# Kernel tuning notes

Measured on AMD Instinct MI355X. Metric: run time of the kernel, lower is better.

## Reference

```python
import jax, jax.numpy as jnp
import numpy as np

B, N, D, YD = 256, 1024, 64, 2
EPS = 1e-7  # keras SCC epsilon clip


def interleave(x):
    # (B, L, ...): out[:,0::2]=first half, out[:,1::2]=second half
    b, L = x.shape[0], x.shape[1]
    a, c = x[:, : L // 2], x[:, L // 2:]
    return jnp.stack([a, c], axis=2).reshape((b, L) + x.shape[2:])


def block_interleave(x, scope):
    # tf.split into N//scope chunks of size `scope`, Interleave each, concat
    b, L = x.shape[0], x.shape[1]
    rest = x.shape[2:]
    xr = x.reshape((b, L // scope, 2, scope // 2) + rest)
    xr = jnp.swapaxes(xr, 2, 3)
    return xr.reshape((b, L) + rest)


def split_even_odd(x):
    # returns (odd, even) = (x[:,0::2], x[:,1::2])
    return x[:, 0::2], x[:, 1::2]


def mlp2(x, W1, b1, W2, b2):
    return jnp.dot(jax.nn.relu(jnp.dot(x, W1) + b1), W2) + b2


def emb2llr(e, W, b):
    return jax.nn.softmax(jnp.dot(e, W) + b, axis=-1)


def scce(v, p):
    # v: (B,L,1) int labels, p: (B,L,2) probs -> (B,L) per-element NLL
    pt = jnp.take_along_axis(p, v, axis=-1)[..., 0]
    return -jnp.log(jnp.clip(pt, EPS, 1.0))


def setup_inputs() -> dict:
    key = jax.random.key(0)
    ks = jax.random.split(key, 16)
    s = lambda fan: 1.0 / np.sqrt(fan)
    return {
        "x": jax.random.randint(ks[0], (B, N, 1), 0, 2, dtype=jnp.int32),
        "y": jax.random.normal(ks[1], (B, N, YD), dtype=jnp.float32),
        "emb_W": jax.random.normal(ks[2], (YD, D), dtype=jnp.float32) * s(YD),
        "emb_b": jnp.zeros((D,), jnp.float32),
        "lab_emb": jax.random.normal(ks[3], (2, D), dtype=jnp.float32) * s(D),
        "cn_W1": jax.random.normal(ks[4], (2 * D, D), dtype=jnp.float32) * s(2 * D),
        "cn_b1": jnp.zeros((D,), jnp.float32),
        "cn_W2": jax.random.normal(ks[5], (D, D), dtype=jnp.float32) * s(D),
        "cn_b2": jnp.zeros((D,), jnp.float32),
        "bn_W1": jax.random.normal(ks[6], (3 * D, D), dtype=jnp.float32) * s(3 * D),
        "bn_b1": jnp.zeros((D,), jnp.float32),
        "bn_W2": jax.random.normal(ks[7], (D, D), dtype=jnp.float32) * s(D),
        "bn_b2": jnp.zeros((D,), jnp.float32),
        "llr_W": jax.random.normal(ks[8], (D, 2), dtype=jnp.float32) * s(D),
        "llr_b": jnp.zeros((2,), jnp.float32),
    }


def reference(x, y, emb_W, emb_b, lab_emb, cn_W1, cn_b1, cn_W2, cn_b2,
              bn_W1, bn_b1, bn_W2, bn_b2, llr_W, llr_b):
    v = x.astype(jnp.int32)  # (B,N,1)
    e = jnp.dot(y, emb_W) + emb_b  # (B,N,D) observation embedding

    losses, preds, norms = [], [], []
    pred = emb2llr(e, llr_W, llr_b)
    losses.append(scce(v, pred))
    preds.append(pred)
    norms.append(jnp.linalg.norm(e, axis=-1))

    scope = 2
    while scope <= N:
        v_il = block_interleave(v, scope)
        v_odd, v_even = split_even_odd(v_il)
        v_xor = jnp.mod(v_odd + v_even, 2)  # (B,N/2,1)
        v_prime = interleave(jnp.concatenate((v_xor, v_even), axis=1))

        e_il = block_interleave(e, scope)
        e_odd, e_even = split_even_odd(e_il)  # (B,N/2,D) each
        v_xor_emb = lab_emb[v_xor[..., 0]]  # (B,N/2,D)

        e1_left = mlp2(jnp.concatenate((e_odd, e_even), axis=-1),
                       cn_W1, cn_b1, cn_W2, cn_b2)
        e1_right = mlp2(jnp.concatenate((e_odd, e_even, v_xor_emb), axis=-1),
                        bn_W1, bn_b1, bn_W2, bn_b2)
        e_prime = interleave(jnp.concatenate((e1_left, e1_right), axis=1))

        pred = emb2llr(e_prime, llr_W, llr_b)
        losses.append(scce(v_prime, pred))
        preds.append(pred)
        norms.append(jnp.linalg.norm(e_prime, axis=-1))

        v, e = v_prime, e_prime
        scope *= 2

    return (jnp.stack(losses, axis=-2),   # (B, S, N)
            jnp.stack(preds, axis=-2),    # (B, N, S, 2)
            jnp.stack(norms, axis=-2))    # (B, S, N)
```

## Files before the change

kernel.cpp:

```cpp
#include <hip/hip_runtime.h>
#include <hip/hip_bf16.h>

#define NB 256
#define NN 1024
#define NSTAGES 11
#define EPSF 1e-7f

typedef unsigned short u16;
typedef unsigned int u32;
typedef unsigned long long u64;
typedef __attribute__((ext_vector_type(8))) short short8;
typedef __attribute__((ext_vector_type(16))) float f32x16;

static constexpr size_t PRED_BASE = (size_t)NB * NSTAGES * NN;
static constexpr size_t NORM_BASE = PRED_BASE + (size_t)NB * NN * NSTAGES * 2;

static constexpr int LW_OFF = 24576;

#define WLDS_FR 30
#define NWREG (48 - WLDS_FR)

static constexpr size_t STAGE_OFF = 131072;
static constexpr size_t PRED_F2_PER_B = (size_t)NSTAGES * NN;

__device__ __forceinline__ u16 f2bf(float f) {
  unsigned u = __float_as_uint(f);
  unsigned r = (u + 0x7fffu + ((u >> 16) & 1u)) >> 16;
  return (u16)r;
}
__device__ __forceinline__ unsigned pack_bf2(float a, float b) {
  __hip_bfloat162 h = __float22bfloat162_rn(make_float2(a, b));
  return *(unsigned*)&h;
}
__device__ __forceinline__ u32 spread16(u32 v) {
  v = (v | (v << 8)) & 0x00FF00FFu;
  v = (v | (v << 4)) & 0x0F0F0F0Fu;
  v = (v | (v << 2)) & 0x33333333u;
  v = (v | (v << 1)) & 0x55555555u;
  return v;
}
template <bool STAGED>
__device__ __forceinline__ void emit_out(float* __restrict__ out, float* __restrict__ pred_ws,
                                         int b, int n, int s,
                                         float z0, float z1, float nrm2, int label) {
  float m  = fmaxf(z0, z1);
  float p0 = expf(z0 - m), p1 = expf(z1 - m);
  float inv = 1.0f / (p0 + p1);
  p0 *= inv; p1 *= inv;
  float pt = label ? p1 : p0;
  pt = fminf(fmaxf(pt, EPSF), 1.0f);
  out[((size_t)b * NSTAGES + s) * NN + n] = -logf(pt);
  if (STAGED) {
    ((float2*)pred_ws)[((size_t)b * NSTAGES + s) * NN + n] = make_float2(p0, p1);
  } else {
    size_t pb = PRED_BASE + (((size_t)b * NN + n) * NSTAGES + s) * 2;
    out[pb + 0] = p0;
    out[pb + 1] = p1;
  }
  out[NORM_BASE + ((size_t)b * NSTAGES + s) * NN + n] = sqrtf(nrm2);
}

__device__ __forceinline__ int eaddr(int row, int c16) {
  return row * 64 + (((c16) ^ (row & 7)) << 3);
}
__device__ __forceinline__ int eaddr32(int row, int m31) {
  return row * 64 + (((((m31) >> 2) ^ (row & 7)) << 3) | (((m31) & 3) << 1));
}

__global__ __launch_bounds__(256) void prep_kernel(
    const float* __restrict__ cn_W1, const float* __restrict__ bn_W1,
    const float* __restrict__ cn_W2, const float* __restrict__ bn_W2,
    const float* __restrict__ lab_emb, const float* __restrict__ llr_W,
    const float* __restrict__ bn_b1,
    u16* __restrict__ wfrag, float* __restrict__ labW_g) {
  int t = blockIdx.x * 256 + threadIdx.x;
  if (t < 3072) {
    int f = t >> 6, l = t & 63, h = l >> 5, c = l & 31;
    const float* src; int ks, nt;
    if (f < 16)      { src = cn_W1; ks = f >> 1; nt = f & 1; }
    else if (f < 32) { int g = f - 16; src = bn_W1; ks = g >> 1; nt = g & 1; }
    else if (f < 40) { int g = f - 32; src = cn_W2; ks = g >> 1; nt = g & 1; }
    else             { int g = f - 40; src = bn_W2; ks = g >> 1; nt = g & 1; }
    int col = 2 * c + nt;
    u16 vals[8];
    #pragma unroll
    for (int j = 0; j < 8; ++j) {
      int k = ks * 16 + h * 8 + j;
      vals[j] = f2bf(src[k * 64 + col]);
    }
    uint4 u;
    u.x = (unsigned)vals[0] | ((unsigned)vals[1] << 16);
    u.y = (unsigned)vals[2] | ((unsigned)vals[3] << 16);
    u.z = (unsigned)vals[4] | ((unsigned)vals[5] << 16);
    u.w = (unsigned)vals[6] | ((unsigned)vals[7] << 16);
    *(uint4*)(wfrag + (size_t)t * 8) = u;
  } else if (t < 3136) {
    int k = t - 3072;
    unsigned wv = (unsigned)f2bf(llr_W[k * 2]) | ((unsigned)f2bf(llr_W[k * 2 + 1]) << 16);
    ((unsigned*)(wfrag + LW_OFF))[k] = wv;
  } else if (t < 3264) {
    int idx = t - 3136;
    int v = idx >> 6, c = idx & 63;
    float acc = bn_b1[c];
    for (int d = 0; d < 64; ++d)
      acc = fmaf(lab_emb[v * 64 + d], bn_W1[(128 + d) * 64 + c], acc);
    labW_g[idx] = acc;
  }
}

__global__ __launch_bounds__(512) void pred_transpose_kernel(
    const float* __restrict__ pred_ws, float* __restrict__ out) {
  __shared__ float2 tb[NSTAGES * 1026];
  const int tid = threadIdx.x;
  const int b = blockIdx.x;
  const float2* src = (const float2*)pred_ws + (size_t)b * PRED_F2_PER_B;
  for (int i = tid; i < NSTAGES * NN; i += 512) {
    int s = i >> 10, n = i & (NN - 1);
    tb[s * 1026 + n] = src[i];
  }
  __syncthreads();
  float2* dst = (float2*)(out + PRED_BASE) + (size_t)b * PRED_F2_PER_B;
  for (int j = tid; j < NSTAGES * NN; j += 512) {
    int n = j / NSTAGES, s = j - n * NSTAGES;
    dst[j] = tb[s * 1026 + n];
  }
}

#define BFR(FI) (((FI) < WLDS_FR) ? *(const short8*)(wlds + (FI) * 512 + ln * 8) \
                                  : Wreg[(FI) - WLDS_FR])

template <int STAGED>
__global__ __launch_bounds__(512, 2) void polar_kernel(
    const int* __restrict__ x, const float* __restrict__ y,
    const float* __restrict__ emb_W, const float* __restrict__ emb_b,
    const u16* __restrict__ wfrag, const float* __restrict__ labW_g,
    const float* __restrict__ cn_b1, const float* __restrict__ cn_b2,
    const float* __restrict__ bn_b2, const float* __restrict__ llr_W,
    const float* __restrict__ llr_b, float* __restrict__ pred_ws,
    float* __restrict__ out) {
  __shared__ __align__(16) u16 eL[NN * 64];
  __shared__ __align__(16) u16 wlds[WLDS_FR * 512];
  __shared__ u32 lwL[64];
  __shared__ u32 vmask[2][32];
  __shared__ float labW[2][64];

  const int tid = threadIdx.x;
  const int w = tid >> 6, ln = tid & 63;
  const int m31 = ln & 31, h8 = ln >> 5;
  const int b = blockIdx.x;

  for (int i = tid; i < WLDS_FR * 64; i += 512)
    ((uint4*)wlds)[i] = ((const uint4*)wfrag)[i];
  if (tid < 64) lwL[tid] = ((const u32*)(wfrag + LW_OFF))[tid];
  if (tid < 128) ((float*)labW)[tid] = labW_g[tid];

  short8 Wreg[NWREG];
  #pragma unroll
  for (int fi = 0; fi < NWREG; ++fi)
    Wreg[fi] = *(const short8*)(wfrag + (size_t)(WLDS_FR + fi) * 512 + ln * 8);

  const float lb0 = llr_b[0], lb1 = llr_b[1];
  const float2 cb1 = *(const float2*)(cn_b1 + 2 * m31);
  const float2 cb2 = *(const float2*)(cn_b2 + 2 * m31);
  const float2 bb2 = *(const float2*)(bn_b2 + 2 * m31);

  #pragma unroll
  for (int rep = 0; rep < 2; ++rep) {
    int n = rep * 512 + tid;
    float2 yv = *(const float2*)(y + ((size_t)b * NN + n) * 2);
    float z0 = lb0, z1 = lb1, nr = 0.f;
    #pragma unroll
    for (int o8 = 0; o8 < 8; ++o8) {
      u32 vals[4];
      #pragma unroll
      for (int jj = 0; jj < 4; ++jj) {
        int o = o8 * 8 + jj * 2;
        float e0 = fmaf(yv.x, emb_W[o],     fmaf(yv.y, emb_W[64 + o],     emb_b[o]));
        float e1 = fmaf(yv.x, emb_W[o + 1], fmaf(yv.y, emb_W[64 + o + 1], emb_b[o + 1]));
        vals[jj] = pack_bf2(e0, e1);
        z0 = fmaf(e0, llr_W[o * 2 + 0], z0); z1 = fmaf(e0, llr_W[o * 2 + 1], z1);
        nr = fmaf(e0, e0, nr);
        z0 = fmaf(e1, llr_W[o * 2 + 2], z0); z1 = fmaf(e1, llr_W[o * 2 + 3], z1);
        nr = fmaf(e1, e1, nr);
      }
      uint4 q; q.x = vals[0]; q.y = vals[1]; q.z = vals[2]; q.w = vals[3];
      *(uint4*)(eL + eaddr(n, o8)) = q;
    }
    int v = x[(size_t)b * NN + n] & 1;
    emit_out<STAGED != 0>(out, pred_ws, b, n, 0, z0, z1, nr, v);
    u64 bm = __ballot(v != 0);
    if (ln == 0)  vmask[0][rep * 16 + 2 * w]     = (u32)bm;
    if (ln == 32) vmask[0][rep * 16 + 2 * w + 1] = (u32)(bm >> 32);
  }
  __syncthreads();

  const float2 lwv0 = *(const float2*)(&labW[0][2 * m31]);
  const float2 lwv1 = *(const float2*)(&labW[1][2 * m31]);

  #pragma unroll 1
  for (int s = 1; s <= 10; ++s) {
    const int sh = s - 1;
    const int half = 1 << sh;
    const u32* vmR = vmask[(s - 1) & 1];
    u32* vmW = vmask[s & 1];

    short8 Ao[2][4], Ae[2][4];
    int io[2], ie[2], vo[2], ve[2], vx[2];
    u32 bxs[2];
    #pragma unroll
    for (int t = 0; t < 2; ++t) {
      int i = 64 * w + 32 * t + m31;
      int g = i >> sh, u = i & (half - 1);
      io[t] = g * (half << 1) + u;
      ie[t] = io[t] + half;
      #pragma unroll
      for (int f = 0; f < 4; ++f) {
        Ao[t][f] = *(const short8*)(eL + eaddr(io[t], f * 2 + h8));
        Ae[t][f] = *(const short8*)(eL + eaddr(ie[t], f * 2 + h8));
      }
      vo[t] = (vmR[io[t] >> 5] >> (io[t] & 31)) & 1;
      ve[t] = (vmR[ie[t] >> 5] >> (ie[t] & 31)) & 1;
      vx[t] = vo[t] ^ ve[t];
      u32 bx = (u32)__ballot(vx[t] != 0);
      u32 be = (u32)__ballot(ve[t] != 0);
      bxs[t] = bx;
      u32 lo = spread16(bx & 0xffffu) | (spread16(be & 0xffffu) << 1);
      u32 hi = spread16(bx >> 16) | (spread16(be >> 16) << 1);
      if (ln == 0) { vmW[4 * w + 2 * t] = lo; vmW[4 * w + 2 * t + 1] = hi; }
    }
    __syncthreads();

    if (s >= 2) {
      const uint4* lwq = (const uint4*)lwL;
      uint4 lq[4][2];
      #pragma unroll
      for (int f = 0; f < 4; ++f) {
        lq[f][0] = lwq[f * 4 + h8 * 2];
        lq[f][1] = lwq[f * 4 + h8 * 2 + 1];
      }
      #pragma unroll
      for (int t = 0; t < 2; ++t) {
        #pragma unroll
        for (int side = 0; side < 2; ++side) {
          float z0 = 0.f, z1 = 0.f, nr = 0.f;
          #pragma unroll
          for (int f = 0; f < 4; ++f) {
            short8 av8 = side ? Ae[t][f] : Ao[t][f];
            #pragma unroll
            for (int j = 0; j < 8; ++j) {
              u32 pv = ((const u32*)&av8)[j >> 1];
              float val = __uint_as_float((j & 1) ? (pv & 0xffff0000u) : (pv << 16));
              u32 lwp = (j < 4) ? ((const u32*)&lq[f][0])[j] : ((const u32*)&lq[f][1])[j - 4];
              z0 = fmaf(val, __uint_as_float(lwp << 16), z0);
              z1 = fmaf(val, __uint_as_float(lwp & 0xffff0000u), z1);
              nr = fmaf(val, val, nr);
            }
          }
          z0 += __shfl_xor(z0, 32);
          z1 += __shfl_xor(z1, 32);
          nr += __shfl_xor(nr, 32);
          if (h8 == 0)
            emit_out<STAGED != 0>(out, pred_ws, b, side ? ie[t] : io[t], s - 1,
                                  z0 + lb0, z1 + lb1, nr, side ? ve[t] : vo[t]);
        }
      }
    }

    f32x16 a0[2], a1[2];
    #pragma unroll
    for (int t = 0; t < 2; ++t)
      #pragma unroll
      for (int r = 0; r < 16; ++r) { a0[t][r] = cb1.x; a1[t][r] = cb1.y; }
    #pragma unroll
    for (int ks = 0; ks < 8; ++ks) {
      short8 B0 = BFR(ks * 2 + 0);
      short8 B1 = BFR(ks * 2 + 1);
      #pragma unroll
      for (int t = 0; t < 2; ++t) {
        short8 a = (ks < 4) ? Ao[t][ks] : Ae[t][ks - 4];
        a0[t] = __builtin_amdgcn_mfma_f32_32x32x16_bf16(a, B0, a0[t], 0, 0, 0);
        a1[t] = __builtin_amdgcn_mfma_f32_32x32x16_bf16(a, B1, a1[t], 0, 0, 0);
      }
    }
    #pragma unroll
    for (int t = 0; t < 2; ++t) {
      int obase = 128 * w + 64 * t;
      #pragma unroll
      for (int r = 0; r < 16; ++r) {
        int row = (r & 3) + 8 * (r >> 2) + 4 * h8;
        int R = obase + 2 * row;
        *(u32*)(eL + eaddr32(R, m31)) =
            pack_bf2(fmaxf(a0[t][r], 0.f), fmaxf(a1[t][r], 0.f));
      }
    }

    #pragma unroll
    for (int t = 0; t < 2; ++t)
      #pragma unroll
      for (int r = 0; r < 16; ++r) {
        int row = (r & 3) + 8 * (r >> 2) + 4 * h8;
        int bit = (bxs[t] >> row) & 1;
        a0[t][r] = bit ? lwv1.x : lwv0.x;
        a1[t][r] = bit ? lwv1.y : lwv0.y;
      }
    #pragma unroll
    for (int ks = 0; ks < 8; ++ks) {
      short8 B0 = BFR(16 + ks * 2 + 0);
      short8 B1 = BFR(16 + ks * 2 + 1);
      #pragma unroll
      for (int t = 0; t < 2; ++t) {
        short8 a = (ks < 4) ? Ao[t][ks] : Ae[t][ks - 4];
        a0[t] = __builtin_amdgcn_mfma_f32_32x32x16_bf16(a, B0, a0[t], 0, 0, 0);
        a1[t] = __builtin_amdgcn_mfma_f32_32x32x16_bf16(a, B1, a1[t], 0, 0, 0);
      }
    }
    #pragma unroll
    for (int t = 0; t < 2; ++t) {
      int obase = 128 * w + 64 * t;
      #pragma unroll
      for (int r = 0; r < 16; ++r) {
        int row = (r & 3) + 8 * (r >> 2) + 4 * h8;
        int R = obase + 2 * row + 1;
        *(u32*)(eL + eaddr32(R, m31)) =
            pack_bf2(fmaxf(a0[t][r], 0.f), fmaxf(a1[t][r], 0.f));
      }
    }

    {
      short8 Hc[2][4];
      #pragma unroll
      for (int t = 0; t < 2; ++t) {
        int R = 128 * w + 64 * t + 2 * m31;
        #pragma unroll
        for (int f = 0; f < 4; ++f)
          Hc[t][f] = *(const short8*)(eL + eaddr(R, f * 2 + h8));
      }
      f32x16 d0[2], d1[2];
      #pragma unroll
      for (int t = 0; t < 2; ++t)
        #pragma unroll
        for (int r = 0; r < 16; ++r) { d0[t][r] = cb2.x; d1[t][r] = cb2.y; }
      #pragma unroll
      for (int ks = 0; ks < 4; ++ks) {
        short8 B0 = BFR(32 + ks * 2 + 0);
        short8 B1 = BFR(32 + ks * 2 + 1);
        #pragma unroll
        for (int t = 0; t < 2; ++t) {
          d0[t] = __builtin_amdgcn_mfma_f32_32x32x16_bf16(Hc[t][ks], B0, d0[t], 0, 0, 0);
          d1[t] = __builtin_amdgcn_mfma_f32_32x32x16_bf16(Hc[t][ks], B1, d1[t], 0, 0, 0);
        }
      }
      #pragma unroll
      for (int t = 0; t < 2; ++t) {
        int obase = 128 * w + 64 * t;
        #pragma unroll
        for (int r = 0; r < 16; ++r) {
          int row = (r & 3) + 8 * (r >> 2) + 4 * h8;
          int R = obase + 2 * row;
          *(u32*)(eL + eaddr32(R, m31)) = pack_bf2(d0[t][r], d1[t][r]);
        }
      }
    }

    {
      short8 Hb[2][4];
      #pragma unroll
      for (int t = 0; t < 2; ++t) {
        int R = 128 * w + 64 * t + 2 * m31 + 1;
        #pragma unroll
        for (int f = 0; f < 4; ++f)
          Hb[t][f] = *(const short8*)(eL + eaddr(R, f * 2 + h8));
      }
      f32x16 d0[2], d1[2];
      #pragma unroll
      for (int t = 0; t < 2; ++t)
        #pragma unroll
        for (int r = 0; r < 16; ++r) { d0[t][r] = bb2.x; d1[t][r] = bb2.y; }
      #pragma unroll
      for (int ks = 0; ks < 4; ++ks) {
        short8 B0 = BFR(40 + ks * 2 + 0);
        short8 B1 = BFR(40 + ks * 2 + 1);
        #pragma unroll
        for (int t = 0; t < 2; ++t) {
          d0[t] = __builtin_amdgcn_mfma_f32_32x32x16_bf16(Hb[t][ks], B0, d0[t], 0, 0, 0);
          d1[t] = __builtin_amdgcn_mfma_f32_32x32x16_bf16(Hb[t][ks], B1, d1[t], 0, 0, 0);
        }
      }
      #pragma unroll
      for (int t = 0; t < 2; ++t) {
        int obase = 128 * w + 64 * t;
        #pragma unroll
        for (int r = 0; r < 16; ++r) {
          int row = (r & 3) + 8 * (r >> 2) + 4 * h8;
          int R = obase + 2 * row + 1;
          *(u32*)(eL + eaddr32(R, m31)) = pack_bf2(d0[t][r], d1[t][r]);
        }
      }
    }
    __syncthreads();
  }

  {
    const uint4* lwq = (const uint4*)lwL;
    uint4 lq[4][2];
    #pragma unroll
    for (int f = 0; f < 4; ++f) {
      lq[f][0] = lwq[f * 4 + h8 * 2];
      lq[f][1] = lwq[f * 4 + h8 * 2 + 1];
    }
    #pragma unroll
    for (int it = 0; it < 4; ++it) {
      int n = 128 * w + 32 * it + m31;
      float z0 = 0.f, z1 = 0.f, nr = 0.f;
      #pragma unroll
      for (int f = 0; f < 4; ++f) {
        short8 av8 = *(const short8*)(eL + eaddr(n, f * 2 + h8));
        #pragma unroll
        for (int j = 0; j < 8; ++j) {
          u32 pv = ((const u32*)&av8)[j >> 1];
          float val = __uint_as_float((j & 1) ? (pv & 0xffff0000u) : (pv << 16));
          u32 lwp = (j < 4) ? ((const u32*)&lq[f][0])[j] : ((const u32*)&lq[f][1])[j - 4];
          z0 = fmaf(val, __uint_as_float(lwp << 16), z0);
          z1 = fmaf(val, __uint_as_float(lwp & 0xffff0000u), z1);
          nr = fmaf(val, val, nr);
        }
      }
      z0 += __shfl_xor(z0, 32);
      z1 += __shfl_xor(z1, 32);
      nr += __shfl_xor(nr, 32);
      int lab = (vmask[0][n >> 5] >> (n & 31)) & 1;
      if (h8 == 0)
        emit_out<STAGED != 0>(out, pred_ws, b, n, NSTAGES - 1, z0 + lb0, z1 + lb1, nr, lab);
    }
  }
}

extern "C" void kernel_launch(void* const* d_in, const int* in_sizes, int n_in,
                              void* d_out, int out_size, void* d_ws, size_t ws_size,
                              hipStream_t stream) {
  const int*   x      = (const int*)d_in[0];
  const float* y      = (const float*)d_in[1];
  const float* emb_W  = (const float*)d_in[2];
  const float* emb_b  = (const float*)d_in[3];
  const float* labemb = (const float*)d_in[4];
  const float* cn_W1  = (const float*)d_in[5];
  const float* cn_b1  = (const float*)d_in[6];
  const float* cn_W2  = (const float*)d_in[7];
  const float* cn_b2  = (const float*)d_in[8];
  const float* bn_W1  = (const float*)d_in[9];
  const float* bn_b1  = (const float*)d_in[10];
  const float* bn_W2  = (const float*)d_in[11];
  const float* bn_b2  = (const float*)d_in[12];
  const float* llr_W  = (const float*)d_in[13];
  const float* llr_b  = (const float*)d_in[14];
  float* out = (float*)d_out;

  u16* wfrag = (u16*)d_ws;
  float* labW_g = (float*)((char*)d_ws + 65536);
  float* pred_ws = (float*)((char*)d_ws + STAGE_OFF);
  size_t need = STAGE_OFF + (size_t)NB * NSTAGES * NN * 2 * sizeof(float);

  prep_kernel<<<13, 256, 0, stream>>>(cn_W1, bn_W1, cn_W2, bn_W2, labemb, llr_W,
                                      bn_b1, wfrag, labW_g);
  if (ws_size >= need) {
    polar_kernel<1><<<NB, 512, 0, stream>>>(x, y, emb_W, emb_b, wfrag, labW_g,
                                            cn_b1, cn_b2, bn_b2, llr_W, llr_b,
                                            pred_ws, out);
    pred_transpose_kernel<<<NB, 512, 0, stream>>>(pred_ws, out);
  } else {
    polar_kernel<0><<<NB, 512, 0, stream>>>(x, y, emb_W, emb_b, wfrag, labW_g,
                                            cn_b1, cn_b2, bn_b2, llr_W, llr_b,
                                            pred_ws, out);
  }
}
```

Baseline: 265.2 us.

## Use 1024-thread blocks with one row-tile per wave, read spilled weights from global

Doubles the block size from 512 to 1024 threads so each wave handles a single 32-row tile per stage instead of two, halving per-thread accumulator and fragment register state. The weight fragments previously held in registers (those not in LDS) are now loaded from global memory on each use. This aims at more waves per block to hide latency in the serial stage loop. The cost is repeated global/L2 reads of the weight fragments each stage, and with one 1024-thread block per CU there is less cross-block overlap than two 512-thread blocks.

```diff
diff --git a/kernel.cpp b/kernel.cpp
--- a/kernel.cpp
+++ b/kernel.cpp
@@ -18,7 +18,6 @@
 static constexpr int LW_OFF = 24576;
 
 #define WLDS_FR 30
-#define NWREG (48 - WLDS_FR)
 
 static constexpr size_t STAGE_OFF = 131072;
 static constexpr size_t PRED_F2_PER_B = (size_t)NSTAGES * NN;
@@ -127,10 +126,10 @@
 }
 
 #define BFR(FI) (((FI) < WLDS_FR) ? *(const short8*)(wlds + (FI) * 512 + ln * 8) \
-                                  : Wreg[(FI) - WLDS_FR])
+                                  : *(const short8*)(wfrag + (size_t)(FI) * 512 + ln * 8))
 
 template <int STAGED>
-__global__ __launch_bounds__(512, 2) void polar_kernel(
+__global__ __launch_bounds__(1024) void polar_kernel(
     const int* __restrict__ x, const float* __restrict__ y,
     const float* __restrict__ emb_W, const float* __restrict__ emb_b,
     const u16* __restrict__ wfrag, const float* __restrict__ labW_g,
@@ -149,24 +148,18 @@
   const int m31 = ln & 31, h8 = ln >> 5;
   const int b = blockIdx.x;
 
-  for (int i = tid; i < WLDS_FR * 64; i += 512)
+  for (int i = tid; i < WLDS_FR * 64; i += 1024)
     ((uint4*)wlds)[i] = ((const uint4*)wfrag)[i];
   if (tid < 64) lwL[tid] = ((const u32*)(wfrag + LW_OFF))[tid];
   if (tid < 128) ((float*)labW)[tid] = labW_g[tid];
-
-  short8 Wreg[NWREG];
-  #pragma unroll
-  for (int fi = 0; fi < NWREG; ++fi)
-    Wreg[fi] = *(const short8*)(wfrag + (size_t)(WLDS_FR + fi) * 512 + ln * 8);
 
   const float lb0 = llr_b[0], lb1 = llr_b[1];
   const float2 cb1 = *(const float2*)(cn_b1 + 2 * m31);
   const float2 cb2 = *(const float2*)(cn_b2 + 2 * m31);
   const float2 bb2 = *(const float2*)(bn_b2 + 2 * m31);
 
-  #pragma unroll
-  for (int rep = 0; rep < 2; ++rep) {
-    int n = rep * 512 + tid;
+  {
+    int n = tid;
     float2 yv = *(const float2*)(y + ((size_t)b * NN + n) * 2);
     float z0 = lb0, z1 = lb1, nr = 0.f;
     #pragma unroll
@@ -189,8 +182,8 @@
     int v = x[(size_t)b * NN + n] & 1;
     emit_out<STAGED != 0>(out, pred_ws, b, n, 0, z0, z1, nr, v);
     u64 bm = __ballot(v != 0);
-    if (ln == 0)  vmask[0][rep * 16 + 2 * w]     = (u32)bm;
-    if (ln == 32) vmask[0][rep * 16 + 2 * w + 1] = (u32)(bm >> 32);
+    if (ln == 0)  vmask[0][2 * w]     = (u32)bm;
+    if (ln == 32) vmask[0][2 * w + 1] = (u32)(bm >> 32);
   }
   __syncthreads();
 
@@ -204,29 +197,28 @@
     const u32* vmR = vmask[(s - 1) & 1];
     u32* vmW = vmask[s & 1];
 
-    short8 Ao[2][4], Ae[2][4];
-    int io[2], ie[2], vo[2], ve[2], vx[2];
-    u32 bxs[2];
-    #pragma unroll
-    for (int t = 0; t < 2; ++t) {
-      int i = 64 * w + 32 * t + m31;
+    short8 Ao[4], Ae[4];
+    int io, ie, vo, ve, vx;
+    u32 bxs;
+    {
+      int i = 32 * w + m31;
       int g = i >> sh, u = i & (half - 1);
-      io[t] = g * (half << 1) + u;
-      ie[t] = io[t] + half;
+      io = g * (half << 1) + u;
+      ie = io + half;
       #pragma unroll
       for (int f = 0; f < 4; ++f) {
-        Ao[t][f] = *(const short8*)(eL + eaddr(io[t], f * 2 + h8));
-        Ae[t][f] = *(const short8*)(eL + eaddr(ie[t], f * 2 + h8));
-      }
-      vo[t] = (vmR[io[t] >> 5] >> (io[t] & 31)) & 1;
-      ve[t] = (vmR[ie[t] >> 5] >> (ie[t] & 31)) & 1;
-      vx[t] = vo[t] ^ ve[t];
-      u32 bx = (u32)__ballot(vx[t] != 0);
-      u32 be = (u32)__ballot(ve[t] != 0);
-      bxs[t] = bx;
+        Ao[f] = *(const short8*)(eL + eaddr(io, f * 2 + h8));
+        Ae[f] = *(const short8*)(eL + eaddr(ie, f * 2 + h8));
+      }
+      vo = (vmR[io >> 5] >> (io & 31)) & 1;
+      ve = (vmR[ie >> 5] >> (ie & 31)) & 1;
+      vx = vo ^ ve;
+      u32 bx = (u32)__ballot(vx != 0);
+      u32 be = (u32)__ballot(ve != 0);
+      bxs = bx;
       u32 lo = spread16(bx & 0xffffu) | (spread16(be & 0xffffu) << 1);
       u32 hi = spread16(bx >> 16) | (spread16(be >> 16) << 1);
-      if (ln == 0) { vmW[4 * w + 2 * t] = lo; vmW[4 * w + 2 * t + 1] = hi; }
+      if (ln == 0) { vmW[2 * w] = lo; vmW[2 * w + 1] = hi; }
     }
     __syncthreads();
 
@@ -239,162 +231,129 @@
         lq[f][1] = lwq[f * 4 + h8 * 2 + 1];
       }
       #pragma unroll
-      for (int t = 0; t < 2; ++t) {
+      for (int side = 0; side < 2; ++side) {
+        float z0 = 0.f, z1 = 0.f, nr = 0.f;
         #pragma unroll
-        for (int side = 0; side < 2; ++side) {
-          float z0 = 0.f, z1 = 0.f, nr = 0.f;
+        for (int f = 0; f < 4; ++f) {
+          short8 av8 = side ? Ae[f] : Ao[f];
           #pragma unroll
-          for (int f = 0; f < 4; ++f) {
-            short8 av8 = side ? Ae[t][f] : Ao[t][f];
-            #pragma unroll
-            for (int j = 0; j < 8; ++j) {
-              u32 pv = ((const u32*)&av8)[j >> 1];
-              float val = __uint_as_float((j & 1) ? (pv & 0xffff0000u) : (pv << 16));
-              u32 lwp = (j < 4) ? ((const u32*)&lq[f][0])[j] : ((const u32*)&lq[f][1])[j - 4];
-              z0 = fmaf(val, __uint_as_float(lwp << 16), z0);
-              z1 = fmaf(val, __uint_as_float(lwp & 0xffff0000u), z1);
-              nr = fmaf(val, val, nr);
-            }
+          for (int j = 0; j < 8; ++j) {
+            u32 pv = ((const u32*)&av8)[j >> 1];
+            float val = __uint_as_float((j & 1) ? (pv & 0xffff0000u) : (pv << 16));
+            u32 lwp = (j < 4) ? ((const u32*)&lq[f][0])[j] : ((const u32*)&lq[f][1])[j - 4];
+            z0 = fmaf(val, __uint_as_float(lwp << 16), z0);
+            z1 = fmaf(val, __uint_as_float(lwp & 0xffff0000u), z1);
+            nr = fmaf(val, val, nr);
           }
-          z0 += __shfl_xor(z0, 32);
-          z1 += __shfl_xor(z1, 32);
-          nr += __shfl_xor(nr, 32);
-          if (h8 == 0)
-            emit_out<STAGED != 0>(out, pred_ws, b, side ? ie[t] : io[t], s - 1,
-                                  z0 + lb0, z1 + lb1, nr, side ? ve[t] : vo[t]);
         }
-      }
-    }
-
-    f32x16 a0[2], a1[2];
-    #pragma unroll
-    for (int t = 0; t < 2; ++t)
-      #pragma unroll
-      for (int r = 0; r < 16; ++r) { a0[t][r] = cb1.x; a1[t][r] = cb1.y; }
+        z0 += __shfl_xor(z0, 32);
+        z1 += __shfl_xor(z1, 32);
+        nr += __shfl_xor(nr, 32);
+        if (h8 == 0)
+          emit_out<STAGED != 0>(out, pred_ws, b, side ? ie : io, s - 1,
+                                z0 + lb0, z1 + lb1, nr, side ? ve : vo);
+      }
+    }
+
+    f32x16 a0, a1;
+    #pragma unroll
+    for (int r = 0; r < 16; ++r) { a0[r] = cb1.x; a1[r] = cb1.y; }
     #pragma unroll
     for (int ks = 0; ks < 8; ++ks) {
       short8 B0 = BFR(ks * 2 + 0);
       short8 B1 = BFR(ks * 2 + 1);
-      #pragma unroll
-      for (int t = 0; t < 2; ++t) {
-        short8 a = (ks < 4) ? Ao[t][ks] : Ae[t][ks - 4];
-        a0[t] = __builtin_amdgcn_mfma_f32_32x32x16_bf16(a, B0, a0[t], 0, 0, 0);
-        a1[t] = __builtin_amdgcn_mfma_f32_32x32x16_bf16(a, B1, a1[t], 0, 0, 0);
-      }
-    }
-    #pragma unroll
-    for (int t = 0; t < 2; ++t) {
-      int obase = 128 * w + 64 * t;
+      short8 a = (ks < 4) ? Ao[ks] : Ae[ks - 4];
+      a0 = __builtin_amdgcn_mfma_f32_32x32x16_bf16(a, B0, a0, 0, 0, 0);
+      a1 = __builtin_amdgcn_mfma_f32_32x32x16_bf16(a, B1, a1, 0, 0, 0);
+    }
+    {
+      int obase = 64 * w;
       #pragma unroll
       for (int r = 0; r < 16; ++r) {
         int row = (r & 3) + 8 * (r >> 2) + 4 * h8;
         int R = obase + 2 * row;
         *(u32*)(eL + eaddr32(R, m31)) =
-            pack_bf2(fmaxf(a0[t][r], 0.f), fmaxf(a1[t][r], 0.f));
-      }
-    }
-
-    #pragma unroll
-    for (int t = 0; t < 2; ++t)
-      #pragma unroll
-      for (int r = 0; r < 16; ++r) {
-        int row = (r & 3) + 8 * (r >> 2) + 4 * h8;
-        int bit = (bxs[t] >> row) & 1;
-        a0[t][r] = bit ? lwv1.x : lwv0.x;
-        a1[t][r] = bit ? lwv1.y : lwv0.y;
-      }
+            pack_bf2(fmaxf(a0[r], 0.f), fmaxf(a1[r], 0.f));
+      }
+    }
+
+    #pragma unroll
+    for (int r = 0; r < 16; ++r) {
+      int row = (r & 3) + 8 * (r >> 2) + 4 * h8;
+      int bit = (bxs >> row) & 1;
+      a0[r] = bit ? lwv1.x : lwv0.x;
+      a1[r] = bit ? lwv1.y : lwv0.y;
+    }
     #pragma unroll
     for (int ks = 0; ks < 8; ++ks) {
       short8 B0 = BFR(16 + ks * 2 + 0);
       short8 B1 = BFR(16 + ks * 2 + 1);
-      #pragma unroll
-      for (int t = 0; t < 2; ++t) {
-        short8 a = (ks < 4) ? Ao[t][ks] : Ae[t][ks - 4];
-        a0[t] = __builtin_amdgcn_mfma_f32_32x32x16_bf16(a, B0, a0[t], 0, 0, 0);
-        a1[t] = __builtin_amdgcn_mfma_f32_32x32x16_bf16(a, B1, a1[t], 0, 0, 0);
-      }
-    }
-    #pragma unroll
-    for (int t = 0; t < 2; ++t) {
-      int obase = 128 * w + 64 * t;
+      short8 a = (ks < 4) ? Ao[ks] : Ae[ks - 4];
+      a0 = __builtin_amdgcn_mfma_f32_32x32x16_bf16(a, B0, a0, 0, 0, 0);
+      a1 = __builtin_amdgcn_mfma_f32_32x32x16_bf16(a, B1, a1, 0, 0, 0);
+    }
+    {
+      int obase = 64 * w;
       #pragma unroll
       for (int r = 0; r < 16; ++r) {
         int row = (r & 3) + 8 * (r >> 2) + 4 * h8;
         int R = obase + 2 * row + 1;
         *(u32*)(eL + eaddr32(R, m31)) =
-            pack_bf2(fmaxf(a0[t][r], 0.f), fmaxf(a1[t][r], 0.f));
+            pack_bf2(fmaxf(a0[r], 0.f), fmaxf(a1[r], 0.f));
       }
     }
 
     {
-      short8 Hc[2][4];
-      #pragma unroll
-      for (int t = 0; t < 2; ++t) {
-        int R = 128 * w + 64 * t + 2 * m31;
+      short8 Hc[4];
+      {
+        int R = 64 * w + 2 * m31;
         #pragma unroll
         for (int f = 0; f < 4; ++f)
-          Hc[t][f] = *(const short8*)(eL + eaddr(R, f * 2 + h8));
-      }
-      f32x16 d0[2], d1[2];
-      #pragma unroll
-      for (int t = 0; t < 2; ++t)
-        #pragma unroll
-        for (int r = 0; r < 16; ++r) { d0[t][r] = cb2.x; d1[t][r] = cb2.y; }
+          Hc[f] = *(const short8*)(eL + eaddr(R, f * 2 + h8));
+      }
+      f32x16 d0, d1;
+      #pragma unroll
+      for (int r = 0; r < 16; ++r) { d0[r] = cb2.x; d1[r] = cb2.y; }
       #pragma unroll
       for (int ks = 0; ks < 4; ++ks) {
         short8 B0 = BFR(32 + ks * 2 + 0);
         short8 B1 = BFR(32 + ks * 2 + 1);
-        #pragma unroll
-        for (int t = 0; t < 2; ++t) {
-          d0[t] = __builtin_amdgcn_mfma_f32_32x32x16_bf16(Hc[t][ks], B0, d0[t], 0, 0, 0);
-          d1[t] = __builtin_amdgcn_mfma_f32_32x32x16_bf16(Hc[t][ks], B1, d1[t], 0, 0, 0);
-        }
-      }
-      #pragma unroll
-      for (int t = 0; t < 2; ++t) {
-        int obase = 128 * w + 64 * t;
-        #pragma unroll
-        for (int r = 0; r < 16; ++r) {
-          int row = (r & 3) + 8 * (r >> 2) + 4 * h8;
-          int R = obase + 2 * row;
-          *(u32*)(eL + eaddr32(R, m31)) = pack_bf2(d0[t][r], d1[t][r]);
-        }
+        d0 = __builtin_amdgcn_mfma_f32_32x32x16_bf16(Hc[ks], B0, d0, 0, 0, 0);
+        d1 = __builtin_amdgcn_mfma_f32_32x32x16_bf16(Hc[ks], B1, d1, 0, 0, 0);
+      }
+      int obase = 64 * w;
+      #pragma unroll
+      for (int r = 0; r < 16; ++r) {
+        int row = (r & 3) + 8 * (r >> 2) + 4 * h8;
+        int R = obase + 2 * row;
+        *(u32*)(eL + eaddr32(R, m31)) = pack_bf2(d0[r], d1[r]);
       }
     }
 
     {
-      short8 Hb[2][4];
-      #pragma unroll
-      for (int t = 0; t < 2; ++t) {
-        int R = 128 * w + 64 * t + 2 * m31 + 1;
+      short8 Hb[4];
+      {
+        int R = 64 * w + 2 * m31 + 1;
         #pragma unroll
         for (int f = 0; f < 4; ++f)
-          Hb[t][f] = *(const short8*)(eL + eaddr(R, f * 2 + h8));
-      }
-      f32x16 d0[2], d1[2];
-      #pragma unroll
-      for (int t = 0; t < 2; ++t)
-        #pragma unroll
-        for (int r = 0; r < 16; ++r) { d0[t][r] = bb2.x; d1[t][r] = bb2.y; }
+          Hb[f] = *(const short8*)(eL + eaddr(R, f * 2 + h8));
+      }
+      f32x16 d0, d1;
+      #pragma unroll
+      for (int r = 0; r < 16; ++r) { d0[r] = bb2.x; d1[r] = bb2.y; }
       #pragma unroll
       for (int ks = 0; ks < 4; ++ks) {
         short8 B0 = BFR(40 + ks * 2 + 0);
         short8 B1 = BFR(40 + ks * 2 + 1);
-        #pragma unroll
-        for (int t = 0; t < 2; ++t) {
-          d0[t] = __builtin_amdgcn_mfma_f32_32x32x16_bf16(Hb[t][ks], B0, d0[t], 0, 0, 0);
-          d1[t] = __builtin_amdgcn_mfma_f32_32x32x16_bf16(Hb[t][ks], B1, d1[t], 0, 0, 0);
-        }
-      }
-      #pragma unroll
-      for (int t = 0; t < 2; ++t) {
-        int obase = 128 * w + 64 * t;
-        #pragma unroll
-        for (int r = 0; r < 16; ++r) {
-          int row = (r & 3) + 8 * (r >> 2) + 4 * h8;
-          int R = obase + 2 * row + 1;
-          *(u32*)(eL + eaddr32(R, m31)) = pack_bf2(d0[t][r], d1[t][r]);
-        }
+        d0 = __builtin_amdgcn_mfma_f32_32x32x16_bf16(Hb[ks], B0, d0, 0, 0, 0);
+        d1 = __builtin_amdgcn_mfma_f32_32x32x16_bf16(Hb[ks], B1, d1, 0, 0, 0);
+      }
+      int obase = 64 * w;
+      #pragma unroll
+      for (int r = 0; r < 16; ++r) {
+        int row = (r & 3) + 8 * (r >> 2) + 4 * h8;
+        int R = obase + 2 * row + 1;
+        *(u32*)(eL + eaddr32(R, m31)) = pack_bf2(d0[r], d1[r]);
       }
     }
     __syncthreads();
@@ -409,8 +368,8 @@
       lq[f][1] = lwq[f * 4 + h8 * 2 + 1];
     }
     #pragma unroll
-    for (int it = 0; it < 4; ++it) {
-      int n = 128 * w + 32 * it + m31;
+    for (int it = 0; it < 2; ++it) {
+      int n = 64 * w + 32 * it + m31;
       float z0 = 0.f, z1 = 0.f, nr = 0.f;
       #pragma unroll
       for (int f = 0; f < 4; ++f) {
@@ -463,13 +422,13 @@
   prep_kernel<<<13, 256, 0, stream>>>(cn_W1, bn_W1, cn_W2, bn_W2, labemb, llr_W,
                                       bn_b1, wfrag, labW_g);
   if (ws_size >= need) {
-    polar_kernel<1><<<NB, 512, 0, stream>>>(x, y, emb_W, emb_b, wfrag, labW_g,
-                                            cn_b1, cn_b2, bn_b2, llr_W, llr_b,
-                                            pred_ws, out);
+    polar_kernel<1><<<NB, 1024, 0, stream>>>(x, y, emb_W, emb_b, wfrag, labW_g,
+                                             cn_b1, cn_b2, bn_b2, llr_W, llr_b,
+                                             pred_ws, out);
     pred_transpose_kernel<<<NB, 512, 0, stream>>>(pred_ws, out);
   } else {
-    polar_kernel<0><<<NB, 512, 0, stream>>>(x, y, emb_W, emb_b, wfrag, labW_g,
-                                            cn_b1, cn_b2, bn_b2, llr_W, llr_b,
-                                            pred_ws, out);
-  }
-}
+    polar_kernel<0><<<NB, 1024, 0, stream>>>(x, y, emb_W, emb_b, wfrag, labW_g,
+                                             cn_b1, cn_b2, bn_b2, llr_W, llr_b,
+                                             pred_ws, out);
+  }
+}
```

Result: slower. 508.5 us (+91.7%).
